# Performance work log

Measured on AMD Instinct MI355X. Metric: run time of the kernel, lower is better.

## Reference

```python
import jax, jax.numpy as jnp
import numpy as np
import math

IN_DIM = 2048
OUT_DIM = 1152
SEQ_LEN = 8
WAY = 5
SHOT = 5
N_QUERIES = 100
MAX_LEN = int(SEQ_LEN * 1.5)
PE_SCALE = 0.1


def make_pe():
    pe = np.zeros((MAX_LEN, IN_DIM), dtype=np.float32)
    position = np.arange(0, MAX_LEN)[:, None].astype(np.float32)
    div_term = np.exp(np.arange(0, IN_DIM, 2).astype(np.float32) * -(math.log(10000.0) / IN_DIM))
    pe[:, 0::2] = np.sin(position * div_term) * PE_SCALE
    pe[:, 1::2] = np.cos(position * div_term) * PE_SCALE
    return jnp.asarray(pe)


def setup_inputs() -> dict:
    key = jax.random.key(0)
    ks = jax.random.split(key, 12)
    support_set = jax.random.normal(ks[0], (WAY * SHOT, SEQ_LEN, IN_DIM), dtype=jnp.float32)
    queries = jax.random.normal(ks[1], (N_QUERIES, SEQ_LEN, IN_DIM), dtype=jnp.float32)
    # labels: each class 0..WAY-1 appears SHOT times (sorted)
    support_labels = jnp.sort(jnp.arange(WAY * SHOT) % WAY)
    s = 1.0 / math.sqrt(IN_DIM)
    def lin(k):
        kw, kb = jax.random.split(k)
        W = jax.random.uniform(kw, (OUT_DIM, IN_DIM), minval=-s, maxval=s, dtype=jnp.float32)
        b = jax.random.uniform(kb, (OUT_DIM,), minval=-s, maxval=s, dtype=jnp.float32)
        return W, b
    sk_W, sk_b = lin(ks[2])
    sv_W, sv_b = lin(ks[3])
    qk_W, qk_b = lin(ks[4])
    qv_W, qv_b = lin(ks[5])
    return {
        "support_set": support_set,
        "support_labels": support_labels,
        "queries": queries,
        "sk_W": sk_W, "sk_b": sk_b,
        "sv_W": sv_W, "sv_b": sv_b,
        "qk_W": qk_W, "qk_b": qk_b,
        "qv_W": qv_W, "qv_b": qv_b,
        "ln_k_g": jnp.ones((OUT_DIM,), jnp.float32),
        "ln_k_b": jnp.zeros((OUT_DIM,), jnp.float32),
        "pe_table": make_pe(),
    }


def layer_norm(x, g, b, eps=1e-5):
    mu = jnp.mean(x, axis=-1, keepdims=True)
    var = jnp.var(x, axis=-1, keepdims=True)
    return (x - mu) / jnp.sqrt(var + eps) * g + b


def reference(support_set, support_labels, queries, sk_W, sk_b, sv_W, sv_b,
              qk_W, qk_b, qv_W, qv_b, ln_k_g, ln_k_b, pe_table):
    n_q, L, _ = queries.shape
    support_set = support_set + pe_table[None, :L]
    queries = queries + pe_table[None, :L]

    s_ks = layer_norm(support_set @ sk_W.T + sk_b, ln_k_g, ln_k_b)  # [S, L, D]
    q_ks = layer_norm(queries @ qk_W.T + qk_b, ln_k_g, ln_k_b)      # [Q, L, D]
    s_vs = support_set @ sv_W.T + sv_b                               # [S, L, D]
    q_vs = queries @ qv_W.T + qv_b                                   # [Q, L, D]

    D = q_ks.shape[-1]
    # group support by class: labels are sorted with equal shots per class
    k_bs = support_set.shape[0] // WAY
    class_k = s_ks.reshape(WAY, k_bs, L, D)   # [C, k, L, D]
    class_v = s_vs.reshape(WAY, k_bs, L, D)

    # scores: [C, Q, L(query), k*L(support)]
    scores = jnp.einsum('qld,ckmd->cqlkm', q_ks, class_k) / math.sqrt(D)
    scores = scores.reshape(WAY, n_q, L, k_bs * L)
    attn = jax.nn.softmax(scores, axis=-1)  # softmax over support frames per query frame
    attn = attn.reshape(WAY, n_q, L, k_bs, L).transpose(0, 1, 3, 2, 4)  # [C,Q,k,L,L]
    proto = jnp.einsum('cqklm,ckmd->cqld', attn, class_v)  # sum over k folded in

    diff = q_vs[None] - proto  # [C, Q, L, D]
    distance = jnp.sum(diff * diff, axis=(-2, -1)) / math.sqrt(D * L)  # [C, Q]
    return -distance.T  # [Q, C]
```

## Files before the change

### kernel.cpp

```cpp
#include <hip/hip_runtime.h>
#include <hip/hip_bf16.h>
#include <math.h>

#define WAY     5
#define NQ      100
#define SEQL    8
#define IN_DIM  2048
#define OUT_DIM 1152
#define QROWS   800
#define SROWS   200
#define QPAD    896
#define SPAD    256

#define OFF_SKB  0
#define OFF_SVB  1152
#define OFF_QKB  2304
#define OFF_QVB  3456
#define OFF_LNG  4608
#define OFF_LNB  5760
#define OFF_RSQ  6912
#define F32_END  7808

#define U_AQ   0
#define U_AS   (U_AQ  + QPAD*IN_DIM)
#define U_QKB  (U_AS  + SPAD*IN_DIM)
#define U_QVB  (U_QKB + QPAD*OUT_DIM)
#define U_SKB  (U_QVB + QPAD*OUT_DIM)
#define U_SVB  (U_SKB + SPAD*OUT_DIM)
#define SPSZ   (2048*SPAD)
#define U_SP   (U_SVB + SPAD*OUT_DIM)
#define U_W    (U_SP + 4*SPSZ)

typedef __attribute__((ext_vector_type(8))) short short8;
typedef __attribute__((ext_vector_type(4))) float f32x4;

__device__ __forceinline__ float bf2f(unsigned short u) {
    return __uint_as_float(((unsigned int)u) << 16);
}
__device__ __forceinline__ unsigned short f2bf(float f) {
    unsigned int u = __float_as_uint(f);
    return (unsigned short)((u + 0x7fffu + ((u >> 16) & 1u)) >> 16);
}
__device__ __forceinline__ bool sniff_bf16(const void* lng) {
    return *((const unsigned int*)lng) != 0x3F800000u;
}
__device__ __forceinline__ float load_s(const void* p, long idx, bool bf) {
    if (bf) return bf2f(((const unsigned short*)p)[idx]);
    return ((const float*)p)[idx];
}
__device__ __forceinline__ float4 load_v4(const void* p, long idx, bool bf) {
    if (bf) {
        ushort4 v = *((const ushort4*)((const unsigned short*)p + idx));
        return make_float4(bf2f(v.x), bf2f(v.y), bf2f(v.z), bf2f(v.w));
    }
    return *((const float4*)((const float*)p + idx));
}
__device__ __forceinline__ void gl_lds16(const unsigned short* g, unsigned short* l) {
    __builtin_amdgcn_global_load_lds(
        (const __attribute__((address_space(1))) unsigned int*)g,
        (__attribute__((address_space(3))) unsigned int*)l,
        16, 0, 0);
}

#define VMWAIT(N) asm volatile("s_waitcnt vmcnt(" #N ")" ::: "memory")

__global__ void stage_kernel(const void* support, const void* queries,
                             const void* skW, const void* svW,
                             const void* qkW, const void* qvW,
                             const void* skb, const void* svb,
                             const void* qkb, const void* qvb,
                             const void* lng, const void* lnb,
                             const void* pe, float* ws) {
    const bool bf = sniff_bf16(lng);
    unsigned short* ub = (unsigned short*)(ws + F32_END);
    const int tid = blockIdx.x * blockDim.x + threadIdx.x;
    const int stride = gridDim.x * blockDim.x;

    for (int i = tid; i < OUT_DIM; i += stride) {
        ws[OFF_SKB + i] = load_s(skb, i, bf);
        ws[OFF_SVB + i] = load_s(svb, i, bf);
        ws[OFF_QKB + i] = load_s(qkb, i, bf);
        ws[OFF_QVB + i] = load_s(qvb, i, bf);
        ws[OFF_LNG + i] = load_s(lng, i, bf);
        ws[OFF_LNB + i] = load_s(lnb, i, bf);
    }
    for (int i = tid; i < QPAD * (IN_DIM / 4); i += stride) {
        const int row = i >> 9, kc = (i & 511) * 4;
        ushort4 o;
        if (row < QROWS) {
            float4 v = load_v4(queries, (long)row * IN_DIM + kc, bf);
            const float4 p = load_v4(pe, (long)(row & 7) * IN_DIM + kc, bf);
            o.x = f2bf(v.x + p.x); o.y = f2bf(v.y + p.y);
            o.z = f2bf(v.z + p.z); o.w = f2bf(v.w + p.w);
        } else o = make_ushort4(0, 0, 0, 0);
        *(ushort4*)&ub[U_AQ + (long)row * IN_DIM + kc] = o;
    }
    for (int i = tid; i < SPAD * (IN_DIM / 4); i += stride) {
        const int row = i >> 9, kc = (i & 511) * 4;
        ushort4 o;
        if (row < SROWS) {
            float4 v = load_v4(support, (long)row * IN_DIM + kc, bf);
            const float4 p = load_v4(pe, (long)(row & 7) * IN_DIM + kc, bf);
            o.x = f2bf(v.x + p.x); o.y = f2bf(v.y + p.y);
            o.z = f2bf(v.z + p.z); o.w = f2bf(v.w + p.w);
        } else o = make_ushort4(0, 0, 0, 0);
        *(ushort4*)&ub[U_AS + (long)row * IN_DIM + kc] = o;
    }
    if (!bf) {
        const float* Wsrc[4] = {(const float*)qkW, (const float*)qvW,
                                (const float*)skW, (const float*)svW};
        for (int j = 0; j < 4; ++j) {
            unsigned short* dst = ub + U_W + (long)j * OUT_DIM * IN_DIM;
            const float* src = Wsrc[j];
            for (int i = tid; i < OUT_DIM * (IN_DIM / 4); i += stride) {
                const long e = (long)i * 4;
                const float4 v = *(const float4*)(src + e);
                ushort4 o;
                o.x = f2bf(v.x); o.y = f2bf(v.y); o.z = f2bf(v.z); o.w = f2bf(v.w);
                *(ushort4*)&dst[e] = o;
            }
        }
    }
}

__global__ __launch_bounds__(256) void proj_mfma(
        const void* skW, const void* svW, const void* qkW, const void* qvW,
        const void* lng, float* ws) {
    const bool is_bf = sniff_bf16(lng);
    unsigned short* ub = (unsigned short*)(ws + F32_END);

    const int jj = (blockIdx.x & 7) * 81 + (blockIdx.x >> 3);

    int job, nx, my;
    if (jj < 504) { job = jj / 252; const int r = jj % 252; my = r % 14; nx = r / 14; }
    else { const int t2 = jj - 504; job = 2 + t2 / 72; const int r = t2 % 72; my = r % 4; nx = r / 4; }

    const unsigned short* A = (job < 2) ? (ub + U_AQ) : (ub + U_AS);
    unsigned short* outb = (job == 0) ? ub + U_QKB : (job == 1) ? ub + U_QVB
                         : (job == 2) ? ub + U_SKB : ub + U_SVB;
    const float* bias = ws + ((job == 0) ? OFF_QKB : (job == 1) ? OFF_QVB
                            : (job == 2) ? OFF_SKB : OFF_SVB);

    const int r0 = my * 64, n0 = nx * 64;

    __shared__ unsigned short Als[4][64 * 32];
    __shared__ unsigned short Bls[4][64 * 32];

    const int t = threadIdx.x, w = t >> 6, l = t & 63;
    const int wr = w >> 1, wc = w & 1;
    const int fm = l & 15, fq = l >> 4;
    const int srow = l >> 2, schunk = (l & 3) * 8;

    const unsigned short* Ag = A + (size_t)(r0 + w * 16 + srow) * IN_DIM + schunk;
    const unsigned short* Bg;
    if (is_bf) {
        const void* Wv = (job == 0) ? qkW : (job == 1) ? qvW : (job == 2) ? skW : svW;
        Bg = (const unsigned short*)Wv + (size_t)(n0 + w * 16 + srow) * IN_DIM + schunk;
    } else {
        Bg = ub + U_W + (size_t)job * OUT_DIM * IN_DIM
           + (size_t)(n0 + w * 16 + srow) * IN_DIM + schunk;
    }
    const int lofs = (w * 16) * 32;

    f32x4 acc[2][2] = {};

#define PSTAGE(tt) do {                                   \
        const int b_ = (tt) & 3;                          \
        gl_lds16(Ag + (size_t)(tt) * 32, &Als[b_][lofs]); \
        gl_lds16(Bg + (size_t)(tt) * 32, &Bls[b_][lofs]); \
    } while (0)

#define MFMA_CORE(BUF)                                                          \
    {                                                                           \
        short8 af[2], bff[2];                                                   \
        _Pragma("unroll")                                                       \
        for (int i = 0; i < 2; ++i)                                             \
            af[i] = *(const short8*)&Als[BUF][(wr * 32 + i * 16 + fm) * 32 + fq * 8]; \
        _Pragma("unroll")                                                       \
        for (int j = 0; j < 2; ++j)                                             \
            bff[j] = *(const short8*)&Bls[BUF][(wc * 32 + j * 16 + fm) * 32 + fq * 8]; \
        _Pragma("unroll")                                                       \
        for (int i = 0; i < 2; ++i)                                             \
            _Pragma("unroll")                                                   \
            for (int j = 0; j < 2; ++j)                                         \
                acc[i][j] = __builtin_amdgcn_mfma_f32_16x16x32_bf16(            \
                    af[i], bff[j], acc[i][j], 0, 0, 0);                         \
    }

    PSTAGE(0); PSTAGE(1); PSTAGE(2);

    const int T = IN_DIM / 32;
    for (int kt = 0; kt < T; ++kt) {
        if (kt <= T - 3)      VMWAIT(4);
        else if (kt == T - 2) VMWAIT(2);
        else                  VMWAIT(0);
        __builtin_amdgcn_s_barrier();
        __builtin_amdgcn_sched_barrier(0);
        if (kt + 3 < T) PSTAGE(kt + 3);
        MFMA_CORE(kt & 3)
    }
#undef PSTAGE
#undef MFMA_CORE

#pragma unroll
    for (int j = 0; j < 2; ++j) {
        const int col = n0 + wc * 32 + j * 16 + fm;
        const float bv = bias[col];
#pragma unroll
        for (int i = 0; i < 2; ++i) {
            const int rb = r0 + wr * 32 + i * 16 + fq * 4;
            const f32x4 v = acc[i][j];
#pragma unroll
            for (int r = 0; r < 4; ++r)
                outb[(size_t)(rb + r) * OUT_DIM + col] = f2bf(v[r] + bv);
        }
    }
}

__global__ __launch_bounds__(256) void finish_kernel(float* ws) {
    const int row = blockIdx.x;
    unsigned short* ub = (unsigned short*)(ws + F32_END);
    const int tid = threadIdx.x;
    __shared__ float xs[OUT_DIM];
    __shared__ float red[8];

    unsigned short* rp;
    int mode, qrow = 0;
    if (row < 896)       { rp = ub + U_QKB + (size_t)row * OUT_DIM; mode = 0; }
    else if (row < 1152) { rp = ub + U_SKB + (size_t)(row - 896) * OUT_DIM; mode = 0; }
    else                 { rp = ub + U_QVB + (size_t)(row - 1152) * OUT_DIM; mode = 1; qrow = row - 1152; }

    float s = 0.f, s2 = 0.f;
    for (int i = tid; i < OUT_DIM / 8; i += 256) {
        const short8 u = *(const short8*)(rp + i * 8);
#pragma unroll
        for (int k = 0; k < 8; ++k) {
            const float v = bf2f((unsigned short)u[k]);
            s += v;
            s2 = fmaf(v, v, s2);
            if (mode == 0) xs[i * 8 + k] = v;
        }
    }
    for (int o = 32; o > 0; o >>= 1) {
        s  += __shfl_down(s,  o, 64);
        s2 += __shfl_down(s2, o, 64);
    }
    if ((tid & 63) == 0) { red[tid >> 6] = s; red[4 + (tid >> 6)] = s2; }
    __syncthreads();

    if (mode == 0) {
        const float S  = red[0] + red[1] + red[2] + red[3];
        const float S2 = red[4] + red[5] + red[6] + red[7];
        const float mu = S * (1.0f / OUT_DIM);
        const float var = S2 * (1.0f / OUT_DIM) - mu * mu;
        const float rs = rsqrtf(var + 1e-5f);
        const float* g = ws + OFF_LNG;
        const float* bn = ws + OFF_LNB;
        for (int i = tid; i < OUT_DIM; i += 256)
            rp[i] = f2bf((xs[i] - mu) * rs * g[i] + bn[i]);
    } else if (tid == 0) {
        ws[OFF_RSQ + qrow] = red[4] + red[5] + red[6] + red[7];
    }
}

__global__ __launch_bounds__(256) void pair_mfma(float* ws) {
    unsigned short* ub = (unsigned short*)(ws + F32_END);
    const int job = blockIdx.z >> 2;
    const int chunk = blockIdx.z & 3;
    if (job >= 3) return;
    if (job == 2 && blockIdx.y >= 4) return;

    const unsigned short* A;
    const unsigned short* B;
    int rowbase;
    if (job == 0)      { A = ub + U_QKB; B = ub + U_SKB; rowbase = 0; }
    else if (job == 1) { A = ub + U_QVB; B = ub + U_SVB; rowbase = 896; }
    else               { A = ub + U_SVB; B = ub + U_SVB; rowbase = 1792; }
    unsigned short* out = ub + U_SP + (size_t)chunk * SPSZ + (size_t)rowbase * SPAD;

    const int r0 = blockIdx.y * 64;
    const int n0 = blockIdx.x * 64;
    const int kbeg = chunk * 288;

    __shared__ unsigned short Als[4][64 * 32];
    __shared__ unsigned short Bls[4][64 * 32];

    const int t = threadIdx.x, w = t >> 6, l = t & 63;
    const int wr = w >> 1, wc = w & 1;
    const int fm = l & 15, fq = l >> 4;
    const int srow = l >> 2, schunk = (l & 3) * 8;

    const unsigned short* Ag = A + (size_t)(r0 + w * 16 + srow) * OUT_DIM + schunk + kbeg;
    const unsigned short* Bg = B + (size_t)(n0 + w * 16 + srow) * OUT_DIM + schunk + kbeg;
    const int lofs = (w * 16) * 32;

    f32x4 acc[2][2] = {};

#define PSTAGE(tt) do {                                   \
        const int b_ = (tt) & 3;                          \
        gl_lds16(Ag + (size_t)(tt) * 32, &Als[b_][lofs]); \
        gl_lds16(Bg + (size_t)(tt) * 32, &Bls[b_][lofs]); \
    } while (0)

    PSTAGE(0); PSTAGE(1); PSTAGE(2);

    const int T = 9;
    for (int kt = 0; kt < T; ++kt) {
        if (kt <= T - 3)      VMWAIT(4);
        else if (kt == T - 2) VMWAIT(2);
        else                  VMWAIT(0);
        __builtin_amdgcn_s_barrier();
        __builtin_amdgcn_sched_barrier(0);
        if (kt + 3 < T) PSTAGE(kt + 3);

        const int buf = kt & 3;
        short8 af[2], bff[2];
#pragma unroll
        for (int i = 0; i < 2; ++i)
            af[i] = *(const short8*)&Als[buf][(wr * 32 + i * 16 + fm) * 32 + fq * 8];
#pragma unroll
        for (int j = 0; j < 2; ++j)
            bff[j] = *(const short8*)&Bls[buf][(wc * 32 + j * 16 + fm) * 32 + fq * 8];
#pragma unroll
        for (int i = 0; i < 2; ++i)
#pragma unroll
            for (int j = 0; j < 2; ++j)
                acc[i][j] = __builtin_amdgcn_mfma_f32_16x16x32_bf16(
                    af[i], bff[j], acc[i][j], 0, 0, 0);
    }
#undef PSTAGE

#pragma unroll
    for (int j = 0; j < 2; ++j) {
        const int col = n0 + wc * 32 + j * 16 + fm;
#pragma unroll
        for (int i = 0; i < 2; ++i) {
            const int rb = r0 + wr * 32 + i * 16 + fq * 4;
            const f32x4 v = acc[i][j];
#pragma unroll
            for (int r = 0; r < 4; ++r)
                out[(size_t)(rb + r) * SPAD + col] = f2bf(v[r]);
        }
    }
}

__global__ __launch_bounds__(256) void final_kernel(const void* lng, float* ws, void* outp) {
    const bool bf = sniff_bf16(lng);
    const int c = blockIdx.x;
    const int q = blockIdx.y;
    unsigned short* ub = (unsigned short*)(ws + F32_END);
    const unsigned short* P = ub + U_SP;

    __shared__ float sS[SEQL][40];
    __shared__ float sT[SEQL][40];
    __shared__ float sA[SEQL][40];
    __shared__ float sG[40][41];
    __shared__ float red[4];

    const int tid = threadIdx.x;
    const float isd = 0.029462782549439483f;

    for (int i = tid; i < SEQL * 40; i += 256) {
        const int l = i / 40, j = i % 40;
        const size_t rs = (size_t)(q * SEQL + l) * SPAD + c * 40 + j;
        const size_t rt = (size_t)(896 + q * SEQL + l) * SPAD + c * 40 + j;
        float s = 0.f, t = 0.f;
#pragma unroll
        for (int p = 0; p < 4; ++p) {
            s += bf2f(P[(size_t)p * SPSZ + rs]);
            t += bf2f(P[(size_t)p * SPSZ + rt]);
        }
        sS[l][j] = s * isd;
        sT[l][j] = t;
    }
    for (int i = tid; i < 40 * 40; i += 256) {
        const int j = i / 40, j2 = i % 40;
        const size_t rg = (size_t)(1792 + c * 40 + j) * SPAD + c * 40 + j2;
        float g = 0.f;
#pragma unroll
        for (int p = 0; p < 4; ++p) g += bf2f(P[(size_t)p * SPSZ + rg]);
        sG[j][j2] = g;
    }
    __syncthreads();

    if (tid < SEQL) {
        const int l = tid;
        float m = -1e30f;
        for (int j = 0; j < 40; ++j) m = fmaxf(m, sS[l][j]);
        float sum = 0.f;
        for (int j = 0; j < 40; ++j) { float e = __expf(sS[l][j] - m); sA[l][j] = e; sum += e; }
        const float inv = 1.0f / sum;
        for (int j = 0; j < 40; ++j) sA[l][j] *= inv;
    }
    __syncthreads();

    float part = 0.f;
    for (int i = tid; i < SEQL * 40; i += 256) {
        const int l = i / 40, j = i % 40;
        float gs = 0.f;
        for (int j2 = 0; j2 < 40; ++j2) gs = fmaf(sG[j][j2], sA[l][j2], gs);
        part += sA[l][j] * (gs - 2.0f * sT[l][j]);
    }
    for (int o = 32; o > 0; o >>= 1) part += __shfl_down(part, o, 64);
    if ((tid & 63) == 0) red[tid >> 6] = part;
    __syncthreads();

    if (tid == 0) {
        float qn = 0.f;
        for (int l = 0; l < SEQL; ++l) qn += ws[OFF_RSQ + q * SEQL + l];
        const float tot = red[0] + red[1] + red[2] + red[3] + qn;
        const float r = -(tot * (1.0f / 96.0f));
        if (bf) ((__hip_bfloat16*)outp)[q * WAY + c] = __float2bfloat16(r);
        else    ((float*)outp)[q * WAY + c] = r;
    }
}

extern "C" void kernel_launch(void* const* d_in, const int* in_sizes, int n_in,
                              void* d_out, int out_size, void* d_ws, size_t ws_size,
                              hipStream_t stream) {
    const void* support = d_in[0];
    const void* queries = d_in[2];
    const void* skW = d_in[3];  const void* skb = d_in[4];
    const void* svW = d_in[5];  const void* svb = d_in[6];
    const void* qkW = d_in[7];  const void* qkb = d_in[8];
    const void* qvW = d_in[9];  const void* qvb = d_in[10];
    const void* lng = d_in[11]; const void* lnb = d_in[12];
    const void* pe  = d_in[13];
    float* ws = (float*)d_ws;

    stage_kernel<<<dim3(512), dim3(256), 0, stream>>>(
        support, queries, skW, svW, qkW, qvW, skb, svb, qkb, qvb, lng, lnb, pe, ws);
    proj_mfma<<<dim3(648), dim3(256), 0, stream>>>(skW, svW, qkW, qvW, lng, ws);
    finish_kernel<<<dim3(2048), dim3(256), 0, stream>>>(ws);
    pair_mfma<<<dim3(4, 14, 12), dim3(256), 0, stream>>>(ws);
    final_kernel<<<dim3(WAY, NQ), dim3(256), 0, stream>>>(lng, ws, d_out);
}
```

Measured before the change: 168.0 us.

## Fold LayerNorm into score algebra and drop the finish kernel

Removes the separate LayerNorm finish kernel. The projection epilogue now writes the key outputs scaled by gamma and atomically accumulates per-row statistics (sum, sum of squares, gamma-weighted sums) plus value row norms. The final kernel rebuilds the normalized attention scores from the raw dot products with a closed-form correction using per-row mean, rstd and the gamma/beta constants. This saves one launch and a full read/write pass over the key activations, at the cost of atomics in the GEMM epilogue and an E[x²]−μ² variance form that is less numerically stable.

```diff
diff --git a/kernel.cpp b/kernel.cpp
--- a/kernel.cpp
+++ b/kernel.cpp
@@ -19,7 +19,9 @@
 #define OFF_LNG  4608
 #define OFF_LNB  5760
 #define OFF_RSQ  6912
-#define F32_END  7808
+#define OFF_STAT 7808
+#define OFF_CST  12416
+#define F32_END  12432
 
 #define U_AQ   0
 #define U_AS   (U_AQ  + QPAD*IN_DIM)
@@ -75,6 +77,7 @@
     unsigned short* ub = (unsigned short*)(ws + F32_END);
     const int tid = blockIdx.x * blockDim.x + threadIdx.x;
     const int stride = gridDim.x * blockDim.x;
+    __shared__ float cred[12];
 
     for (int i = tid; i < OUT_DIM; i += stride) {
         ws[OFF_SKB + i] = load_s(skb, i, bf);
@@ -83,6 +86,28 @@
         ws[OFF_QVB + i] = load_s(qvb, i, bf);
         ws[OFF_LNG + i] = load_s(lng, i, bf);
         ws[OFF_LNB + i] = load_s(lnb, i, bf);
+    }
+    for (int i = tid; i < 896 + 1152 * 4; i += stride)
+        ws[OFF_RSQ + i] = 0.0f;
+    if (blockIdx.x == 0) {
+        float g2 = 0.f, gb = 0.f, bb = 0.f;
+        for (int i = threadIdx.x; i < OUT_DIM; i += 256) {
+            const float g = load_s(lng, i, bf), b = load_s(lnb, i, bf);
+            g2 = fmaf(g, g, g2); gb = fmaf(g, b, gb); bb = fmaf(b, b, bb);
+        }
+        for (int o = 32; o > 0; o >>= 1) {
+            g2 += __shfl_down(g2, o, 64);
+            gb += __shfl_down(gb, o, 64);
+            bb += __shfl_down(bb, o, 64);
+        }
+        const int wv = threadIdx.x >> 6;
+        if ((threadIdx.x & 63) == 0) { cred[wv] = g2; cred[4 + wv] = gb; cred[8 + wv] = bb; }
+        __syncthreads();
+        if (threadIdx.x == 0) {
+            ws[OFF_CST + 0] = cred[0] + cred[1] + cred[2] + cred[3];
+            ws[OFF_CST + 1] = cred[4] + cred[5] + cred[6] + cred[7];
+            ws[OFF_CST + 2] = cred[8] + cred[9] + cred[10] + cred[11];
+        }
     }
     for (int i = tid; i < QPAD * (IN_DIM / 4); i += stride) {
         const int row = i >> 9, kc = (i & 511) * 4;
@@ -202,64 +227,61 @@
 #undef PSTAGE
 #undef MFMA_CORE
 
-#pragma unroll
-    for (int j = 0; j < 2; ++j) {
-        const int col = n0 + wc * 32 + j * 16 + fm;
-        const float bv = bias[col];
+    const int col0 = n0 + wc * 32 + fm;
+    const int col1 = col0 + 16;
+    const float bv0 = bias[col0], bv1 = bias[col1];
+
+    if (job == 0 || job == 2) {
+        const float g0 = ws[OFF_LNG + col0], g1 = ws[OFF_LNG + col1];
+        const float lb0 = ws[OFF_LNB + col0], lb1 = ws[OFF_LNB + col1];
+        const int sbase = (job == 0) ? 0 : 896;
 #pragma unroll
         for (int i = 0; i < 2; ++i) {
             const int rb = r0 + wr * 32 + i * 16 + fq * 4;
-            const f32x4 v = acc[i][j];
-#pragma unroll
-            for (int r = 0; r < 4; ++r)
-                outb[(size_t)(rb + r) * OUT_DIM + col] = f2bf(v[r] + bv);
-        }
-    }
-}
-
-__global__ __launch_bounds__(256) void finish_kernel(float* ws) {
-    const int row = blockIdx.x;
-    unsigned short* ub = (unsigned short*)(ws + F32_END);
-    const int tid = threadIdx.x;
-    __shared__ float xs[OUT_DIM];
-    __shared__ float red[8];
-
-    unsigned short* rp;
-    int mode, qrow = 0;
-    if (row < 896)       { rp = ub + U_QKB + (size_t)row * OUT_DIM; mode = 0; }
-    else if (row < 1152) { rp = ub + U_SKB + (size_t)(row - 896) * OUT_DIM; mode = 0; }
-    else                 { rp = ub + U_QVB + (size_t)(row - 1152) * OUT_DIM; mode = 1; qrow = row - 1152; }
-
-    float s = 0.f, s2 = 0.f;
-    for (int i = tid; i < OUT_DIM / 8; i += 256) {
-        const short8 u = *(const short8*)(rp + i * 8);
-#pragma unroll
-        for (int k = 0; k < 8; ++k) {
-            const float v = bf2f((unsigned short)u[k]);
-            s += v;
-            s2 = fmaf(v, v, s2);
-            if (mode == 0) xs[i * 8 + k] = v;
-        }
-    }
-    for (int o = 32; o > 0; o >>= 1) {
-        s  += __shfl_down(s,  o, 64);
-        s2 += __shfl_down(s2, o, 64);
-    }
-    if ((tid & 63) == 0) { red[tid >> 6] = s; red[4 + (tid >> 6)] = s2; }
-    __syncthreads();
-
-    if (mode == 0) {
-        const float S  = red[0] + red[1] + red[2] + red[3];
-        const float S2 = red[4] + red[5] + red[6] + red[7];
-        const float mu = S * (1.0f / OUT_DIM);
-        const float var = S2 * (1.0f / OUT_DIM) - mu * mu;
-        const float rs = rsqrtf(var + 1e-5f);
-        const float* g = ws + OFF_LNG;
-        const float* bn = ws + OFF_LNB;
-        for (int i = tid; i < OUT_DIM; i += 256)
-            rp[i] = f2bf((xs[i] - mu) * rs * g[i] + bn[i]);
-    } else if (tid == 0) {
-        ws[OFF_RSQ + qrow] = red[4] + red[5] + red[6] + red[7];
+#pragma unroll
+            for (int r = 0; r < 4; ++r) {
+                const float a0 = acc[i][0][r] + bv0;
+                const float a1 = acc[i][1][r] + bv1;
+                outb[(size_t)(rb + r) * OUT_DIM + col0] = f2bf(a0 * g0);
+                outb[(size_t)(rb + r) * OUT_DIM + col1] = f2bf(a1 * g1);
+                float sx  = a0 + a1;
+                float sx2 = a0 * a0 + a1 * a1;
+                float sp  = a0 * g0 * g0 + a1 * g1 * g1;
+                float sq  = a0 * g0 * lb0 + a1 * g1 * lb1;
+#pragma unroll
+                for (int m = 1; m < 16; m <<= 1) {
+                    sx  += __shfl_xor(sx,  m, 64);
+                    sx2 += __shfl_xor(sx2, m, 64);
+                    sp  += __shfl_xor(sp,  m, 64);
+                    sq  += __shfl_xor(sq,  m, 64);
+                }
+                if (fm == 0) {
+                    float* st = ws + OFF_STAT + (size_t)(sbase + rb + r) * 4;
+                    atomicAdd(st + 0, sx);
+                    atomicAdd(st + 1, sx2);
+                    atomicAdd(st + 2, sp);
+                    atomicAdd(st + 3, sq);
+                }
+            }
+        }
+    } else {
+#pragma unroll
+        for (int i = 0; i < 2; ++i) {
+            const int rb = r0 + wr * 32 + i * 16 + fq * 4;
+#pragma unroll
+            for (int r = 0; r < 4; ++r) {
+                const float a0 = acc[i][0][r] + bv0;
+                const float a1 = acc[i][1][r] + bv1;
+                outb[(size_t)(rb + r) * OUT_DIM + col0] = f2bf(a0);
+                outb[(size_t)(rb + r) * OUT_DIM + col1] = f2bf(a1);
+                if (job == 1) {
+                    float s2 = a0 * a0 + a1 * a1;
+#pragma unroll
+                    for (int m = 1; m < 16; m <<= 1) s2 += __shfl_xor(s2, m, 64);
+                    if (fm == 0) atomicAdd(ws + OFF_RSQ + rb + r, s2);
+                }
+            }
+        }
     }
 }
 
@@ -356,9 +378,26 @@
     __shared__ float sA[SEQL][40];
     __shared__ float sG[40][41];
     __shared__ float red[4];
+    __shared__ float qd[SEQL][4];
+    __shared__ float sd[40][4];
 
     const int tid = threadIdx.x;
     const float isd = 0.029462782549439483f;
+
+    if (tid < SEQL) {
+        const float* st = ws + OFF_STAT + (size_t)(q * SEQL + tid) * 4;
+        const float mu = st[0] * (1.0f / OUT_DIM);
+        const float var = st[1] * (1.0f / OUT_DIM) - mu * mu;
+        qd[tid][0] = mu; qd[tid][1] = rsqrtf(var + 1e-5f);
+        qd[tid][2] = st[2]; qd[tid][3] = st[3];
+    } else if (tid < SEQL + 40) {
+        const int j = tid - SEQL;
+        const float* st = ws + OFF_STAT + (size_t)(896 + c * 40 + j) * 4;
+        const float mu = st[0] * (1.0f / OUT_DIM);
+        const float var = st[1] * (1.0f / OUT_DIM) - mu * mu;
+        sd[j][0] = mu; sd[j][1] = rsqrtf(var + 1e-5f);
+        sd[j][2] = st[2]; sd[j][3] = st[3];
+    }
 
     for (int i = tid; i < SEQL * 40; i += 256) {
         const int l = i / 40, j = i % 40;
@@ -370,7 +409,7 @@
             s += bf2f(P[(size_t)p * SPSZ + rs]);
             t += bf2f(P[(size_t)p * SPSZ + rt]);
         }
-        sS[l][j] = s * isd;
+        sS[l][j] = s;
         sT[l][j] = t;
     }
     for (int i = tid; i < 40 * 40; i += 256) {
@@ -385,8 +424,18 @@
 
     if (tid < SEQL) {
         const int l = tid;
+        const float G2 = ws[OFF_CST + 0], GB = ws[OFF_CST + 1], BB = ws[OFF_CST + 2];
+        const float muq = qd[l][0], rq = qd[l][1], Pq = qd[l][2], Qq = qd[l][3];
+        const float cl = rq * (Qq - muq * GB) + BB;
         float m = -1e30f;
-        for (int j = 0; j < 40; ++j) m = fmaxf(m, sS[l][j]);
+        for (int j = 0; j < 40; ++j) {
+            const float mus = sd[j][0], rs_ = sd[j][1], Ps = sd[j][2], Qs = sd[j][3];
+            float S = rq * rs_ * (sS[l][j] - mus * Pq - muq * Ps + muq * mus * G2)
+                    + cl + rs_ * (Qs - mus * GB);
+            S *= isd;
+            sS[l][j] = S;
+            m = fmaxf(m, S);
+        }
         float sum = 0.f;
         for (int j = 0; j < 40; ++j) { float e = __expf(sS[l][j] - m); sA[l][j] = e; sum += e; }
         const float inv = 1.0f / sum;
@@ -431,7 +480,6 @@
     stage_kernel<<<dim3(512), dim3(256), 0, stream>>>(
         support, queries, skW, svW, qkW, qvW, skb, svb, qkb, qvb, lng, lnb, pe, ws);
     proj_mfma<<<dim3(648), dim3(256), 0, stream>>>(skW, svW, qkW, qvW, lng, ws);
-    finish_kernel<<<dim3(2048), dim3(256), 0, stream>>>(ws);
     pair_mfma<<<dim3(4, 14, 12), dim3(256), 0, stream>>>(ws);
     final_kernel<<<dim3(WAY, NQ), dim3(256), 0, stream>>>(lng, ws, d_out);
 }
```

After: 188.1 us. 1.12x slower.

## Double K-tile depth to 64 and XOR-swizzle LDS layout in projection GEMM

Applied to the files above, without the earlier changes.

Each pipeline stage of the projection GEMM now covers 64 elements of K instead of 32, which halves the number of barrier and wait iterations. Each stage issues four global-to-LDS loads per wave and runs two MFMA sub-steps. The LDS tiles use an XOR swizzle on 16-byte chunks keyed by row, meant to avoid bank conflicts on the wider 128-byte rows. In exchange, LDS use doubles to 64 KB per block, which may lower occupancy, and the wait counts are retuned to match the extra loads in flight.

```diff
diff --git a/kernel.cpp b/kernel.cpp
--- a/kernel.cpp
+++ b/kernel.cpp
@@ -143,56 +143,70 @@
 
     const int r0 = my * 64, n0 = nx * 64;
 
-    __shared__ unsigned short Als[4][64 * 32];
-    __shared__ unsigned short Bls[4][64 * 32];
+    __shared__ unsigned short Als[4][64 * 64];
+    __shared__ unsigned short Bls[4][64 * 64];
 
     const int t = threadIdx.x, w = t >> 6, l = t & 63;
     const int wr = w >> 1, wc = w & 1;
     const int fm = l & 15, fq = l >> 4;
-    const int srow = l >> 2, schunk = (l & 3) * 8;
-
-    const unsigned short* Ag = A + (size_t)(r0 + w * 16 + srow) * IN_DIM + schunk;
+
+    const int sr8 = l >> 3;
+    const int sc  = ((l & 7) ^ sr8) * 8;
+
+    const unsigned short* Ag = A + (size_t)(r0 + w * 16 + sr8) * IN_DIM + sc;
     const unsigned short* Bg;
     if (is_bf) {
         const void* Wv = (job == 0) ? qkW : (job == 1) ? qvW : (job == 2) ? skW : svW;
-        Bg = (const unsigned short*)Wv + (size_t)(n0 + w * 16 + srow) * IN_DIM + schunk;
+        Bg = (const unsigned short*)Wv + (size_t)(n0 + w * 16 + sr8) * IN_DIM + sc;
     } else {
         Bg = ub + U_W + (size_t)job * OUT_DIM * IN_DIM
-           + (size_t)(n0 + w * 16 + srow) * IN_DIM + schunk;
-    }
-    const int lofs = (w * 16) * 32;
+           + (size_t)(n0 + w * 16 + sr8) * IN_DIM + sc;
+    }
+    const int lofs0 = (w * 16) * 64;
+    const int lofs1 = (w * 16 + 8) * 64;
 
     f32x4 acc[2][2] = {};
 
-#define PSTAGE(tt) do {                                   \
-        const int b_ = (tt) & 3;                          \
-        gl_lds16(Ag + (size_t)(tt) * 32, &Als[b_][lofs]); \
-        gl_lds16(Bg + (size_t)(tt) * 32, &Bls[b_][lofs]); \
+#define PSTAGE(tt) do {                                                     \
+        const int b_ = (tt) & 3;                                            \
+        gl_lds16(Ag + (size_t)(tt) * 64,                &Als[b_][lofs0]);   \
+        gl_lds16(Ag + (size_t)8 * IN_DIM + (tt) * 64,   &Als[b_][lofs1]);   \
+        gl_lds16(Bg + (size_t)(tt) * 64,                &Bls[b_][lofs0]);   \
+        gl_lds16(Bg + (size_t)8 * IN_DIM + (tt) * 64,   &Bls[b_][lofs1]);   \
     } while (0)
 
-#define MFMA_CORE(BUF)                                                          \
-    {                                                                           \
-        short8 af[2], bff[2];                                                   \
-        _Pragma("unroll")                                                       \
-        for (int i = 0; i < 2; ++i)                                             \
-            af[i] = *(const short8*)&Als[BUF][(wr * 32 + i * 16 + fm) * 32 + fq * 8]; \
-        _Pragma("unroll")                                                       \
-        for (int j = 0; j < 2; ++j)                                             \
-            bff[j] = *(const short8*)&Bls[BUF][(wc * 32 + j * 16 + fm) * 32 + fq * 8]; \
-        _Pragma("unroll")                                                       \
-        for (int i = 0; i < 2; ++i)                                             \
-            _Pragma("unroll")                                                   \
-            for (int j = 0; j < 2; ++j)                                         \
-                acc[i][j] = __builtin_amdgcn_mfma_f32_16x16x32_bf16(            \
-                    af[i], bff[j], acc[i][j], 0, 0, 0);                         \
+#define MFMA_CORE(BUF)                                                         \
+    {                                                                          \
+        _Pragma("unroll")                                                      \
+        for (int h = 0; h < 2; ++h) {                                          \
+            short8 af[2], bff[2];                                              \
+            _Pragma("unroll")                                                  \
+            for (int i = 0; i < 2; ++i) {                                      \
+                const int rowA = wr * 32 + i * 16 + fm;                        \
+                af[i] = *(const short8*)&Als[BUF][rowA * 64                    \
+                        + ((((h << 2) | fq) ^ (fm & 7)) * 8)];                 \
+            }                                                                  \
+            _Pragma("unroll")                                                  \
+            for (int j = 0; j < 2; ++j) {                                      \
+                const int rowB = wc * 32 + j * 16 + fm;                        \
+                bff[j] = *(const short8*)&Bls[BUF][rowB * 64                   \
+                        + ((((h << 2) | fq) ^ (fm & 7)) * 8)];                 \
+            }                                                                  \
+            _Pragma("unroll")                                                  \
+            for (int i = 0; i < 2; ++i)                                        \
+                _Pragma("unroll")                                              \
+                for (int j = 0; j < 2; ++j)                                    \
+                    acc[i][j] = __builtin_amdgcn_mfma_f32_16x16x32_bf16(       \
+                        af[i], bff[j], acc[i][j], 0, 0, 0);                    \
+        }                                                                      \
     }
 
     PSTAGE(0); PSTAGE(1); PSTAGE(2);
 
-    const int T = IN_DIM / 32;
+    const int T = IN_DIM / 64;
     for (int kt = 0; kt < T; ++kt) {
-        if (kt <= T - 3)      VMWAIT(4);
-        else if (kt == T - 2) VMWAIT(2);
+        if (kt <= T - 3)      VMWAIT(8);
+        else if (kt == T - 2) VMWAIT(4);
         else                  VMWAIT(0);
         __builtin_amdgcn_s_barrier();
         __builtin_amdgcn_sched_barrier(0);
```

After: 178.1 us. +6.0%, slower.

## Split projection GEMM over K into two partials; drop split-K in pair GEMM

Applied to the files above, without the earlier changes.

The projection GEMM now splits the 2048-long reduction into two halves, doubling the block count to 1296 so more CUs stay busy. Each half writes bf16 partials to a new buffer, and finish_kernel sums them, adds the bias, and writes the final Q/K/V rows for all four outputs. In exchange, pair_mfma drops its 4-way K split and runs the full reduction in 3 z-slices, so final_kernel reads a single partial. The cost is an extra partial-buffer round trip, bf16 rounding of the partials before they are summed, and fewer blocks in the pair GEMM.

```diff
diff --git a/kernel.cpp b/kernel.cpp
--- a/kernel.cpp
+++ b/kernel.cpp
@@ -27,9 +27,10 @@
 #define U_QVB  (U_QKB + QPAD*OUT_DIM)
 #define U_SKB  (U_QVB + QPAD*OUT_DIM)
 #define U_SVB  (U_SKB + SPAD*OUT_DIM)
-#define SPSZ   (2048*SPAD)
-#define U_SP   (U_SVB + SPAD*OUT_DIM)
-#define U_W    (U_SP + 4*SPSZ)
+#define PPSZ   (2304*OUT_DIM)
+#define U_PP   (U_SVB + SPAD*OUT_DIM)
+#define U_SP   (U_PP + 2*PPSZ)
+#define U_W    (U_SP + 2048*SPAD)
 
 typedef __attribute__((ext_vector_type(8))) short short8;
 typedef __attribute__((ext_vector_type(4))) float f32x4;
@@ -129,19 +130,24 @@
     const bool is_bf = sniff_bf16(lng);
     unsigned short* ub = (unsigned short*)(ws + F32_END);
 
-    const int jj = (blockIdx.x & 7) * 81 + (blockIdx.x >> 3);
-
-    int job, nx, my;
-    if (jj < 504) { job = jj / 252; const int r = jj % 252; my = r % 14; nx = r / 14; }
-    else { const int t2 = jj - 504; job = 2 + t2 / 72; const int r = t2 % 72; my = r % 4; nx = r / 4; }
+    const int jj = (blockIdx.x & 7) * 162 + (blockIdx.x >> 3);
+
+    int job, nx, my, ch;
+    if (jj < 1008) {
+        job = jj / 504; const int r = jj % 504;
+        my = r % 14; ch = (r / 14) & 1; nx = r / 28;
+    } else {
+        const int t2 = jj - 1008; job = 2 + t2 / 144; const int r = t2 % 144;
+        my = r % 4; ch = (r / 4) & 1; nx = r / 8;
+    }
 
     const unsigned short* A = (job < 2) ? (ub + U_AQ) : (ub + U_AS);
-    unsigned short* outb = (job == 0) ? ub + U_QKB : (job == 1) ? ub + U_QVB
-                         : (job == 2) ? ub + U_SKB : ub + U_SVB;
-    const float* bias = ws + ((job == 0) ? OFF_QKB : (job == 1) ? OFF_QVB
-                            : (job == 2) ? OFF_SKB : OFF_SVB);
+    const int rowbase[4] = {0, 896, 1792, 2048};
+    unsigned short* out = ub + U_PP + (size_t)ch * PPSZ
+                        + (size_t)rowbase[job] * OUT_DIM;
 
     const int r0 = my * 64, n0 = nx * 64;
+    const int kbeg = ch * 1024;
 
     __shared__ unsigned short Als[4][64 * 32];
     __shared__ unsigned short Bls[4][64 * 32];
@@ -151,14 +157,14 @@
     const int fm = l & 15, fq = l >> 4;
     const int srow = l >> 2, schunk = (l & 3) * 8;
 
-    const unsigned short* Ag = A + (size_t)(r0 + w * 16 + srow) * IN_DIM + schunk;
+    const unsigned short* Ag = A + (size_t)(r0 + w * 16 + srow) * IN_DIM + schunk + kbeg;
     const unsigned short* Bg;
     if (is_bf) {
         const void* Wv = (job == 0) ? qkW : (job == 1) ? qvW : (job == 2) ? skW : svW;
-        Bg = (const unsigned short*)Wv + (size_t)(n0 + w * 16 + srow) * IN_DIM + schunk;
+        Bg = (const unsigned short*)Wv + (size_t)(n0 + w * 16 + srow) * IN_DIM + schunk + kbeg;
     } else {
         Bg = ub + U_W + (size_t)job * OUT_DIM * IN_DIM
-           + (size_t)(n0 + w * 16 + srow) * IN_DIM + schunk;
+           + (size_t)(n0 + w * 16 + srow) * IN_DIM + schunk + kbeg;
     }
     const int lofs = (w * 16) * 32;
 
@@ -189,7 +195,7 @@
 
     PSTAGE(0); PSTAGE(1); PSTAGE(2);
 
-    const int T = IN_DIM / 32;
+    const int T = 1024 / 32;
     for (int kt = 0; kt < T; ++kt) {
         if (kt <= T - 3)      VMWAIT(4);
         else if (kt == T - 2) VMWAIT(2);
@@ -205,14 +211,13 @@
 #pragma unroll
     for (int j = 0; j < 2; ++j) {
         const int col = n0 + wc * 32 + j * 16 + fm;
-        const float bv = bias[col];
 #pragma unroll
         for (int i = 0; i < 2; ++i) {
             const int rb = r0 + wr * 32 + i * 16 + fq * 4;
             const f32x4 v = acc[i][j];
 #pragma unroll
             for (int r = 0; r < 4; ++r)
-                outb[(size_t)(rb + r) * OUT_DIM + col] = f2bf(v[r] + bv);
+                out[(size_t)(rb + r) * OUT_DIM + col] = f2bf(v[r]);
         }
     }
 }
@@ -220,27 +225,50 @@
 __global__ __launch_bounds__(256) void finish_kernel(float* ws) {
     const int row = blockIdx.x;
     unsigned short* ub = (unsigned short*)(ws + F32_END);
+    const unsigned short* pp = ub + U_PP + (size_t)row * OUT_DIM;
     const int tid = threadIdx.x;
     __shared__ float xs[OUT_DIM];
     __shared__ float red[8];
 
-    unsigned short* rp;
+    const float* bias;
+    unsigned short* outb;
     int mode, qrow = 0;
-    if (row < 896)       { rp = ub + U_QKB + (size_t)row * OUT_DIM; mode = 0; }
-    else if (row < 1152) { rp = ub + U_SKB + (size_t)(row - 896) * OUT_DIM; mode = 0; }
-    else                 { rp = ub + U_QVB + (size_t)(row - 1152) * OUT_DIM; mode = 1; qrow = row - 1152; }
+    if (row < 896)       { bias = ws + OFF_QKB; outb = ub + U_QKB + (size_t)row * OUT_DIM; mode = 0; }
+    else if (row < 1792) { bias = ws + OFF_QVB; outb = ub + U_QVB + (size_t)(row - 896) * OUT_DIM; mode = 2; qrow = row - 896; }
+    else if (row < 2048) { bias = ws + OFF_SKB; outb = ub + U_SKB + (size_t)(row - 1792) * OUT_DIM; mode = 0; }
+    else                 { bias = ws + OFF_SVB; outb = ub + U_SVB + (size_t)(row - 2048) * OUT_DIM; mode = 1; }
 
     float s = 0.f, s2 = 0.f;
     for (int i = tid; i < OUT_DIM / 8; i += 256) {
-        const short8 u = *(const short8*)(rp + i * 8);
-#pragma unroll
-        for (int k = 0; k < 8; ++k) {
-            const float v = bf2f((unsigned short)u[k]);
-            s += v;
-            s2 = fmaf(v, v, s2);
-            if (mode == 0) xs[i * 8 + k] = v;
-        }
-    }
+        float v[8];
+        {
+            const float4 b0 = *(const float4*)(bias + i * 8);
+            const float4 b1 = *(const float4*)(bias + i * 8 + 4);
+            v[0] = b0.x; v[1] = b0.y; v[2] = b0.z; v[3] = b0.w;
+            v[4] = b1.x; v[5] = b1.y; v[6] = b1.z; v[7] = b1.w;
+        }
+#pragma unroll
+        for (int p = 0; p < 2; ++p) {
+            const short8 u = *(const short8*)(pp + (size_t)p * PPSZ + i * 8);
+#pragma unroll
+            for (int k = 0; k < 8; ++k) v[k] += bf2f((unsigned short)u[k]);
+        }
+        if (mode == 0) {
+#pragma unroll
+            for (int k = 0; k < 8; ++k) {
+                xs[i * 8 + k] = v[k];
+                s += v[k];
+                s2 = fmaf(v[k], v[k], s2);
+            }
+        } else {
+#pragma unroll
+            for (int k = 0; k < 8; ++k) {
+                outb[i * 8 + k] = f2bf(v[k]);
+                s2 = fmaf(v[k], v[k], s2);
+            }
+        }
+    }
+
     for (int o = 32; o > 0; o >>= 1) {
         s  += __shfl_down(s,  o, 64);
         s2 += __shfl_down(s2, o, 64);
@@ -257,17 +285,15 @@
         const float* g = ws + OFF_LNG;
         const float* bn = ws + OFF_LNB;
         for (int i = tid; i < OUT_DIM; i += 256)
-            rp[i] = f2bf((xs[i] - mu) * rs * g[i] + bn[i]);
-    } else if (tid == 0) {
+            outb[i] = f2bf((xs[i] - mu) * rs * g[i] + bn[i]);
+    } else if (mode == 2 && tid == 0) {
         ws[OFF_RSQ + qrow] = red[4] + red[5] + red[6] + red[7];
     }
 }
 
 __global__ __launch_bounds__(256) void pair_mfma(float* ws) {
     unsigned short* ub = (unsigned short*)(ws + F32_END);
-    const int job = blockIdx.z >> 2;
-    const int chunk = blockIdx.z & 3;
-    if (job >= 3) return;
+    const int job = blockIdx.z;
     if (job == 2 && blockIdx.y >= 4) return;
 
     const unsigned short* A;
@@ -276,11 +302,10 @@
     if (job == 0)      { A = ub + U_QKB; B = ub + U_SKB; rowbase = 0; }
     else if (job == 1) { A = ub + U_QVB; B = ub + U_SVB; rowbase = 896; }
     else               { A = ub + U_SVB; B = ub + U_SVB; rowbase = 1792; }
-    unsigned short* out = ub + U_SP + (size_t)chunk * SPSZ + (size_t)rowbase * SPAD;
+    unsigned short* out = ub + U_SP + (size_t)rowbase * SPAD;
 
     const int r0 = blockIdx.y * 64;
     const int n0 = blockIdx.x * 64;
-    const int kbeg = chunk * 288;
 
     __shared__ unsigned short Als[4][64 * 32];
     __shared__ unsigned short Bls[4][64 * 32];
@@ -290,8 +315,8 @@
     const int fm = l & 15, fq = l >> 4;
     const int srow = l >> 2, schunk = (l & 3) * 8;
 
-    const unsigned short* Ag = A + (size_t)(r0 + w * 16 + srow) * OUT_DIM + schunk + kbeg;
-    const unsigned short* Bg = B + (size_t)(n0 + w * 16 + srow) * OUT_DIM + schunk + kbeg;
+    const unsigned short* Ag = A + (size_t)(r0 + w * 16 + srow) * OUT_DIM + schunk;
+    const unsigned short* Bg = B + (size_t)(n0 + w * 16 + srow) * OUT_DIM + schunk;
     const int lofs = (w * 16) * 32;
 
     f32x4 acc[2][2] = {};
@@ -304,7 +329,7 @@
 
     PSTAGE(0); PSTAGE(1); PSTAGE(2);
 
-    const int T = 9;
+    const int T = OUT_DIM / 32;
     for (int kt = 0; kt < T; ++kt) {
         if (kt <= T - 3)      VMWAIT(4);
         else if (kt == T - 2) VMWAIT(2);
@@ -364,22 +389,12 @@
         const int l = i / 40, j = i % 40;
         const size_t rs = (size_t)(q * SEQL + l) * SPAD + c * 40 + j;
         const size_t rt = (size_t)(896 + q * SEQL + l) * SPAD + c * 40 + j;
-        float s = 0.f, t = 0.f;
-#pragma unroll
-        for (int p = 0; p < 4; ++p) {
-            s += bf2f(P[(size_t)p * SPSZ + rs]);
-            t += bf2f(P[(size_t)p * SPSZ + rt]);
-        }
-        sS[l][j] = s * isd;
-        sT[l][j] = t;
+        sS[l][j] = bf2f(P[rs]) * isd;
+        sT[l][j] = bf2f(P[rt]);
     }
     for (int i = tid; i < 40 * 40; i += 256) {
         const int j = i / 40, j2 = i % 40;
-        const size_t rg = (size_t)(1792 + c * 40 + j) * SPAD + c * 40 + j2;
-        float g = 0.f;
-#pragma unroll
-        for (int p = 0; p < 4; ++p) g += bf2f(P[(size_t)p * SPSZ + rg]);
-        sG[j][j2] = g;
+        sG[j][j2] = bf2f(P[(size_t)(1792 + c * 40 + j) * SPAD + c * 40 + j2]);
     }
     __syncthreads();
 
@@ -430,8 +445,8 @@
 
     stage_kernel<<<dim3(512), dim3(256), 0, stream>>>(
         support, queries, skW, svW, qkW, qvW, skb, svb, qkb, qvb, lng, lnb, pe, ws);
-    proj_mfma<<<dim3(648), dim3(256), 0, stream>>>(skW, svW, qkW, qvW, lng, ws);
-    finish_kernel<<<dim3(2048), dim3(256), 0, stream>>>(ws);
-    pair_mfma<<<dim3(4, 14, 12), dim3(256), 0, stream>>>(ws);
+    proj_mfma<<<dim3(1296), dim3(256), 0, stream>>>(skW, svW, qkW, qvW, lng, ws);
+    finish_kernel<<<dim3(2304), dim3(256), 0, stream>>>(ws);
+    pair_mfma<<<dim3(4, 14, 3), dim3(256), 0, stream>>>(ws);
     final_kernel<<<dim3(WAY, NQ), dim3(256), 0, stream>>>(lng, ws, d_out);
 }
```

Measured after the change: 177.6 us. +5.7%, slower.
